# Kernel tuning notes

Measured on AMD Instinct MI355X. Metric: run time of the kernel, lower is better.

Reference implementation:

```python
import jax, jax.numpy as jnp
import numpy as np

B, K, D, H, ZDIM = 65536, 16, 64, 128, 16

def setup_inputs() -> dict:
    key = jax.random.key(0)
    ks = jax.random.split(key, 20)
    s = 0.05
    inp = {
        'z': jax.random.normal(ks[0], (B, ZDIM), dtype=jnp.float32),
        'y': jax.random.randint(ks[1], (B,), 0, K),
        # backbone: 4 fc blocks (Linear+ReLU)
        'bw0': jax.random.normal(ks[2], (ZDIM, H), dtype=jnp.float32) * s,
        'bb0': jnp.zeros((H,), dtype=jnp.float32),
        'bw1': jax.random.normal(ks[3], (H, H), dtype=jnp.float32) * s,
        'bb1': jnp.zeros((H,), dtype=jnp.float32),
        'bw2': jax.random.normal(ks[4], (H, H), dtype=jnp.float32) * s,
        'bb2': jnp.zeros((H,), dtype=jnp.float32),
        'bw3': jax.random.normal(ks[5], (H, H), dtype=jnp.float32) * s,
        'bb3': jnp.zeros((H,), dtype=jnp.float32),
        # K heads, weights stacked on leading expert axis; layers 0-2 have ReLU, layer 3 does not
        'hw0': jax.random.normal(ks[6], (K, H, H), dtype=jnp.float32) * s,
        'hb0': jnp.zeros((K, H), dtype=jnp.float32),
        'hw1': jax.random.normal(ks[7], (K, H, H), dtype=jnp.float32) * s,
        'hb1': jnp.zeros((K, H), dtype=jnp.float32),
        'hw2': jax.random.normal(ks[8], (K, H, H), dtype=jnp.float32) * s,
        'hb2': jnp.zeros((K, H), dtype=jnp.float32),
        'hw3': jax.random.normal(ks[9], (K, H, D), dtype=jnp.float32) * s,
        'hb3': jnp.zeros((K, D), dtype=jnp.float32),
    }
    return inp

def reference(z, y, bw0, bb0, bw1, bb1, bw2, bb2, bw3, bb3,
              hw0, hb0, hw1, hb1, hw2, hb2, hw3, hb3):
    h = jax.nn.relu(z @ bw0 + bb0)
    h = jax.nn.relu(h @ bw1 + bb1)
    h = jax.nn.relu(h @ bw2 + bb2)
    h = jax.nn.relu(h @ bw3 + bb3)          # [B, H]
    # all K expert heads (faithful to original: compute all, then gather)
    a = jax.nn.relu(jnp.einsum('bi,kij->bkj', h, hw0) + hb0)  # [B, K, H]
    a = jax.nn.relu(jnp.einsum('bki,kij->bkj', a, hw1) + hb1)
    a = jax.nn.relu(jnp.einsum('bki,kij->bkj', a, hw2) + hb2)
    a = jnp.einsum('bki,kij->bkj', a, hw3) + hb3              # [B, K, D], no ReLU
    # select the y-th head per sample
    out = jnp.take_along_axis(a, y[:, None, None], axis=1)[:, 0, :]  # [B, D]
    return out
```

## Files before the change

kernel.cpp:

```cpp
#include <hip/hip_runtime.h>
#include <hip/hip_bf16.h>
#include <stdint.h>


typedef _Float16 f16;
typedef __attribute__((ext_vector_type(4)))  _Float16 f16x4;
typedef __attribute__((ext_vector_type(8)))  _Float16 f16x8;
typedef __attribute__((ext_vector_type(16))) float    f32x16;
typedef uint32_t u32;

#define MFMA(a, b, c) __builtin_amdgcn_mfma_f32_32x32x16_f16((a), (b), (c), 0, 0, 0)

constexpr int Bc = 65536;
constexpr int Kc = 16;
constexpr int Hc = 128;
constexpr int Dc = 64;

constexpr int CAP  = 4608;
constexpr int BPE  = CAP / 64;
constexpr int NBLK = Kc * BPE;

constexpr float INV_LOSCALE = 1.0f / 1024.0f;

constexpr int BBW_F16 = 2048 + 3 * 16384;
constexpr int HWE_F16 = 3 * 16384 + 8192;

__device__ __forceinline__ f32x16 zero16() {
    f32x16 z;
#pragma unroll
    for (int i = 0; i < 16; ++i) z[i] = 0.0f;
    return z;
}

__device__ __forceinline__ int actOff(int s, int u) {
    return s * 128 + ((u ^ (s & 15)) << 3);
}

template<bool RELU>
__device__ __forceinline__ void epi_store(
    const f32x16& aH0, const f32x16& aL0,
    const f32x16& aH1, const f32x16& aL1,
    const float* biasLds, f16* aOut, int wid, int l31, int bh)
{
#pragma unroll
    for (int rg = 0; rg < 4; ++rg) {
        const float4 bv = *(const float4*)(biasLds + 32 * wid + 8 * rg + 4 * bh);
        const float bb[4] = {bv.x, bv.y, bv.z, bv.w};
#pragma unroll
        for (int mt = 0; mt < 2; ++mt) {
            const f32x16& aH = mt ? aH1 : aH0;
            const f32x16& aL = mt ? aL1 : aL0;
            f16x4 h4;
#pragma unroll
            for (int j = 0; j < 4; ++j) {
                float v = fmaf(aL[4 * rg + j], INV_LOSCALE, aH[4 * rg + j]) + bb[j];
                if (RELU) v = fmaxf(v, 0.0f);
                h4[j] = (f16)v;
            }
            const int s = 32 * mt + l31;
            *(f16x4*)(aOut + actOff(s, 4 * wid + rg) + 4 * bh) = h4;
        }
    }
}

__device__ __forceinline__ void layer4(
    const f16* __restrict__ Wh, const f16* __restrict__ Wl,
    const float* biasLds, const f16* aIn, f16* aOut,
    int wid, int lane, int l31, int bh)
{
    const f16* ph = Wh + wid * 4096 + lane * 8;
    const f16* pl = Wl + wid * 4096 + lane * 8;

    f32x16 aH0 = zero16(), aH1 = zero16(), aL0 = zero16(), aL1 = zero16();
#pragma unroll
    for (int ks = 0; ks < 8; ++ks) {
        const f16x8 whi = *(const f16x8*)(ph + ks * 512);
        const f16x8 wlo = *(const f16x8*)(pl + ks * 512);
        const f16x8 a0 = *(const f16x8*)(aIn + actOff(l31,      2 * ks + bh));
        const f16x8 a1 = *(const f16x8*)(aIn + actOff(32 + l31, 2 * ks + bh));
        aH0 = MFMA(whi, a0, aH0);
        aH1 = MFMA(whi, a1, aH1);
        aL0 = MFMA(wlo, a0, aL0);
        aL1 = MFMA(wlo, a1, aL1);
    }
    epi_store<true>(aH0, aL0, aH1, aL1, biasLds, aOut, wid, l31, bh);
}

__global__ __launch_bounds__(256, 3) void backbone_mfma(
    const float* __restrict__ z,
    const f16* __restrict__ bbH, const f16* __restrict__ bbL,
    const float* __restrict__ bb0, const float* __restrict__ bb1,
    const float* __restrict__ bb2, const float* __restrict__ bb3,
    f16* __restrict__ hHi)
{
    __shared__ __attribute__((aligned(16))) f16 A[64 * 128];
    __shared__ __attribute__((aligned(16))) f16 B[64 * 128];
    __shared__ __attribute__((aligned(16))) float BIAS[512];

    const int tid = threadIdx.x;
    const int wid = tid >> 6, lane = tid & 63;
    const int l31 = lane & 31, bh = lane >> 5;
    const int s0 = blockIdx.x * 64;

#pragma unroll
    for (int r = 0; r < 2; ++r) {
        const int i = r * 256 + tid;
        float v;
        if      (i < 128) v = bb0[i];
        else if (i < 256) v = bb1[i - 128];
        else if (i < 384) v = bb2[i - 256];
        else              v = bb3[i - 384];
        BIAS[i] = v;
    }

    if (tid < 128) {
        const int m = tid >> 1, hf = tid & 1;
        const float* zp = z + (size_t)(s0 + m) * 16 + hf * 8;
        const float4 a0 = *(const float4*)(zp);
        const float4 a1 = *(const float4*)(zp + 4);
        f16x8 t;
        t[0] = (f16)a0.x; t[1] = (f16)a0.y; t[2] = (f16)a0.z; t[3] = (f16)a0.w;
        t[4] = (f16)a1.x; t[5] = (f16)a1.y; t[6] = (f16)a1.z; t[7] = (f16)a1.w;
        *(f16x8*)(A + actOff(m, hf)) = t;
    }
    __syncthreads();

    {
        const f16x8 w0h = *(const f16x8*)(bbH + wid * 512 + lane * 8);
        const f16x8 w0l = *(const f16x8*)(bbL + wid * 512 + lane * 8);
        const f16x8 a0 = *(const f16x8*)(A + actOff(l31,      bh));
        const f16x8 a1 = *(const f16x8*)(A + actOff(32 + l31, bh));
        f32x16 aH0 = zero16(), aH1 = zero16(), aL0 = zero16(), aL1 = zero16();
        aH0 = MFMA(w0h, a0, aH0);
        aH1 = MFMA(w0h, a1, aH1);
        aL0 = MFMA(w0l, a0, aL0);
        aL1 = MFMA(w0l, a1, aL1);
        epi_store<true>(aH0, aL0, aH1, aL1, BIAS, B, wid, l31, bh);
    }
    __syncthreads();

    layer4(bbH + 2048,  bbL + 2048,  BIAS + 128, B, A, wid, lane, l31, bh);
    __syncthreads();
    layer4(bbH + 18432, bbL + 18432, BIAS + 256, A, B, wid, lane, l31, bh);
    __syncthreads();
    layer4(bbH + 34816, bbL + 34816, BIAS + 384, B, A, wid, lane, l31, bh);
    __syncthreads();

    {
        const int m = tid >> 2, q = tid & 3;
#pragma unroll
        for (int i = 0; i < 4; ++i) {
            const f16x8 v = *(const f16x8*)(A + actOff(m, 4 * q + i));
            *(f16x8*)(hHi + (size_t)(s0 + m) * Hc + q * 32 + i * 8) = v;
        }
    }
}

__global__ void scatter_kernel(const int* __restrict__ y,
                               int* __restrict__ idxb, int* __restrict__ cursor)
{
    __shared__ int lc[Kc];
    __shared__ int lbase[Kc];
    const int tx = threadIdx.x;
    if (tx < Kc) lc[tx] = 0;
    __syncthreads();
    const int b = blockIdx.x * 256 + tx;
    const int e = y[b];
    const int r = atomicAdd(&lc[e], 1);
    __syncthreads();
    if (tx < Kc) lbase[tx] = atomicAdd(&cursor[tx * 16], lc[tx]);
    __syncthreads();
    const int slot = lbase[e] + r;
    if (slot < CAP) idxb[e * CAP + slot] = b;
}

__global__ __launch_bounds__(256, 3) void heads_mfma(
    const f16* hHi,
    const int* __restrict__ idxb, const int* __restrict__ cursor,
    const f16* __restrict__ hH, const f16* __restrict__ hL,
    const float* __restrict__ hb0, const float* __restrict__ hb1,
    const float* __restrict__ hb2, const float* __restrict__ hb3,
    float* out)
{
    __shared__ __attribute__((aligned(16))) f16 A[64 * 128];
    __shared__ __attribute__((aligned(16))) f16 B[64 * 128];
    __shared__ __attribute__((aligned(16))) float BIAS[512];
    __shared__ int sidx[64];

    const int blk = blockIdx.x;
    const int e = blk / BPE;
    const int local0 = (blk % BPE) * 64;
    const int cnt = min(cursor[e * 16], CAP);
    const int nvalid = cnt - local0;
    if (nvalid <= 0) return;

    const int tid = threadIdx.x;
    const int wid = tid >> 6, lane = tid & 63;
    const int l31 = lane & 31, bh = lane >> 5;

#pragma unroll
    for (int r = 0; r < 2; ++r) {
        const int i = r * 256 + tid;
        if (i < 448) {
            float v;
            if      (i < 128) v = hb0[e * Hc + i];
            else if (i < 256) v = hb1[e * Hc + i - 128];
            else if (i < 384) v = hb2[e * Hc + i - 256];
            else              v = hb3[e * Dc + i - 384];
            BIAS[i] = v;
        }
    }
    if (tid < 64) sidx[tid] = (tid < nvalid) ? idxb[e * CAP + local0 + tid] : -1;
    __syncthreads();

    {
        const int m = tid >> 2, q = tid & 3;
        const int b = sidx[m];
        if (b >= 0) {
            const f16* hp = hHi + (size_t)b * Hc + q * 32;
#pragma unroll
            for (int i = 0; i < 4; ++i)
                *(f16x8*)(A + actOff(m, 4 * q + i)) = *(const f16x8*)(hp + i * 8);
        } else {
            f16x8 zz;
#pragma unroll
            for (int j = 0; j < 8; ++j) zz[j] = (f16)0.0f;
#pragma unroll
            for (int i = 0; i < 4; ++i)
                *(f16x8*)(A + actOff(m, 4 * q + i)) = zz;
        }
    }
    __syncthreads();

    const size_t we = (size_t)e * HWE_F16;
    layer4(hH + we,         hL + we,         BIAS,       A, B, wid, lane, l31, bh);
    __syncthreads();
    layer4(hH + we + 16384, hL + we + 16384, BIAS + 128, B, A, wid, lane, l31, bh);
    __syncthreads();
    layer4(hH + we + 32768, hL + we + 32768, BIAS + 256, A, B, wid, lane, l31, bh);
    __syncthreads();

    if (wid < 2) {
        const f16* ph = hH + we + 49152 + wid * 4096 + lane * 8;
        const f16* pl = hL + we + 49152 + wid * 4096 + lane * 8;
        f32x16 aH0 = zero16(), aH1 = zero16(), aL0 = zero16(), aL1 = zero16();
#pragma unroll
        for (int ks = 0; ks < 8; ++ks) {
            const f16x8 whi = *(const f16x8*)(ph + ks * 512);
            const f16x8 wlo = *(const f16x8*)(pl + ks * 512);
            const f16x8 a0 = *(const f16x8*)(B + actOff(l31,      2 * ks + bh));
            const f16x8 a1 = *(const f16x8*)(B + actOff(32 + l31, 2 * ks + bh));
            aH0 = MFMA(whi, a0, aH0);
            aH1 = MFMA(whi, a1, aH1);
            aL0 = MFMA(wlo, a0, aL0);
            aL1 = MFMA(wlo, a1, aL1);
        }
#pragma unroll
        for (int mt = 0; mt < 2; ++mt) {
            const int b = sidx[32 * mt + l31];
            if (b < 0) continue;
            const f32x16& aH = mt ? aH1 : aH0;
            const f32x16& aL = mt ? aL1 : aL0;
#pragma unroll
            for (int rg = 0; rg < 4; ++rg) {
                const int nb = 32 * wid + 8 * rg + 4 * bh;
                const float4 bv = *(const float4*)(BIAS + 384 + nb);
                float4 v;
                v.x = fmaf(aL[4 * rg + 0], INV_LOSCALE, aH[4 * rg + 0]) + bv.x;
                v.y = fmaf(aL[4 * rg + 1], INV_LOSCALE, aH[4 * rg + 1]) + bv.y;
                v.z = fmaf(aL[4 * rg + 2], INV_LOSCALE, aH[4 * rg + 2]) + bv.z;
                v.w = fmaf(aL[4 * rg + 3], INV_LOSCALE, aH[4 * rg + 3]) + bv.w;
                *(float4*)(out + (size_t)b * Dc + nb) = v;
            }
        }
    }
}

__global__ void prep_w(
    const float* __restrict__ bw0, const float* __restrict__ bw1,
    const float* __restrict__ bw2, const float* __restrict__ bw3,
    const float* __restrict__ hw0, const float* __restrict__ hw1,
    const float* __restrict__ hw2, const float* __restrict__ hw3,
    f16* __restrict__ bbH, f16* __restrict__ bbL,
    f16* __restrict__ hH,  f16* __restrict__ hL,
    int* __restrict__ cursor)
{
    __shared__ float T[32][33];
    const int id = blockIdx.x;
    const int tx = threadIdx.x;

    if (id == 0) cursor[tx] = 0;

    const float* src; f16 *dh, *dl;
    int K, N, k0, n0;
    bool big;

    if (id < 52) {
        if (id < 4) {
            src = bw0; dh = bbH; dl = bbL;
            K = 16; N = 128; k0 = 0; n0 = id * 32; big = false;
        } else {
            const int t = id - 4;
            const int l = t / 16, tile = t % 16;
            const float* bws[3] = {bw1, bw2, bw3};
            src = bws[l];
            dh = bbH + 2048 + l * 16384;
            dl = bbL + 2048 + l * 16384;
            K = 128; N = 128; big = true;
            k0 = (tile >> 2) * 32; n0 = (tile & 3) * 32;
        }
    } else {
        const int t = id - 52;
        const int e = t / 56, r = t % 56;
        if (r < 48) {
            const int l = r / 16, tile = r % 16;
            const float* hws[3] = {hw0, hw1, hw2};
            src = hws[l] + (size_t)e * 16384;
            dh = hH + (size_t)e * HWE_F16 + l * 16384;
            dl = hL + (size_t)e * HWE_F16 + l * 16384;
            K = 128; N = 128; big = true;
            k0 = (tile >> 2) * 32; n0 = (tile & 3) * 32;
        } else {
            const int r2 = r - 48;
            src = hw3 + (size_t)e * 8192;
            dh = hH + (size_t)e * HWE_F16 + 49152;
            dl = hL + (size_t)e * HWE_F16 + 49152;
            K = 128; N = 64; big = true;
            k0 = (r2 >> 1) * 32; n0 = (r2 & 1) * 32;
        }
    }

    const int c = tx & 31, g = tx >> 5;
#pragma unroll
    for (int i = 0; i < 4; ++i) {
        const int row = g * 4 + i;
        if (k0 + row < K)
            T[c][row] = src[(size_t)(k0 + row) * N + n0 + c];
    }
    __syncthreads();
#pragma unroll
    for (int i = 0; i < 4; ++i) {
        const int n = n0 + g * 4 + i;
        const int k = k0 + c;
        if (k < K) {
            const float v = T[g * 4 + i][c];
            const f16 hi = (f16)v;
            const f16 lo = (f16)((v - (float)hi) * 1024.0f);
            size_t didx;
            if (big)
                didx = (size_t)(n >> 5) * 4096 + (size_t)(k >> 4) * 512
                     + ((k >> 3) & 1) * 256 + (n & 31) * 8 + (k & 7);
            else
                didx = (size_t)(n >> 5) * 512 + (size_t)(k >> 3) * 256
                     + (n & 31) * 8 + (k & 7);
            dh[didx] = hi;
            dl[didx] = lo;
        }
    }
}

extern "C" void kernel_launch(void* const* d_in, const int* in_sizes, int n_in,
                              void* d_out, int out_size, void* d_ws, size_t ws_size,
                              hipStream_t stream)
{
    const float* z   = (const float*)d_in[0];
    const int*   y   = (const int*)d_in[1];
    const float* bw0 = (const float*)d_in[2];
    const float* bb0 = (const float*)d_in[3];
    const float* bw1 = (const float*)d_in[4];
    const float* bb1 = (const float*)d_in[5];
    const float* bw2 = (const float*)d_in[6];
    const float* bb2 = (const float*)d_in[7];
    const float* bw3 = (const float*)d_in[8];
    const float* bb3 = (const float*)d_in[9];
    const float* hw0 = (const float*)d_in[10];
    const float* hb0 = (const float*)d_in[11];
    const float* hw1 = (const float*)d_in[12];
    const float* hb1 = (const float*)d_in[13];
    const float* hw2 = (const float*)d_in[14];
    const float* hb2 = (const float*)d_in[15];
    const float* hw3 = (const float*)d_in[16];
    const float* hb3 = (const float*)d_in[17];
    float* out = (float*)d_out;

    f16* hHi = (f16*)d_out;

    char* p = (char*)d_ws;
    f16* bbH = (f16*)p;  p += (size_t)BBW_F16 * 2;
    f16* bbL = (f16*)p;  p += (size_t)BBW_F16 * 2;
    f16* hH  = (f16*)p;  p += (size_t)Kc * HWE_F16 * 2;
    f16* hL  = (f16*)p;  p += (size_t)Kc * HWE_F16 * 2;
    int* idxb = (int*)p; p += (size_t)Kc * CAP * 4;
    int* cursor = (int*)p;

    prep_w<<<52 + Kc * 56, 256, 0, stream>>>(bw0, bw1, bw2, bw3,
                                             hw0, hw1, hw2, hw3,
                                             bbH, bbL, hH, hL, cursor);

    scatter_kernel<<<Bc / 256, 256, 0, stream>>>(y, idxb, cursor);

    backbone_mfma<<<Bc / 64, 256, 0, stream>>>(z, bbH, bbL,
                                               bb0, bb1, bb2, bb3, hHi);

    heads_mfma<<<NBLK, 256, 0, stream>>>(hHi, idxb, cursor,
                                         hH, hL, hb0, hb1, hb2, hb3, out);
}
```

Baseline: 154.1 us.

## Fuse backbone and head MLPs into one expert-grouped kernel, merge prep with scatter

The backbone and the selected head now run in one kernel. Samples are gathered by expert up front, so each block loads z rows by index, runs the four backbone layers and then that expert's head layers entirely in LDS. This removes the f16 hidden-state round trip through global memory and one kernel launch. The weight-prep and scatter kernels are merged into a single grid, with the cursor cleared by a memset, to cut another launch. The risk is that per-block bias loads grow, and samples beyond CAP per expert are still dropped as before.

```diff
diff --git a/kernel.cpp b/kernel.cpp
--- a/kernel.cpp
+++ b/kernel.cpp
@@ -24,6 +24,8 @@
 
 constexpr int BBW_F16 = 2048 + 3 * 16384;
 constexpr int HWE_F16 = 3 * 16384 + 8192;
+
+constexpr int PREP_BLKS = 52 + Kc * 56;
 
 __device__ __forceinline__ f32x16 zero16() {
     f32x16 z;
@@ -86,42 +88,63 @@
     epi_store<true>(aH0, aL0, aH1, aL1, biasLds, aOut, wid, l31, bh);
 }
 
-__global__ __launch_bounds__(256, 3) void backbone_mfma(
+__global__ __launch_bounds__(256, 3) void fused_mlp(
     const float* __restrict__ z,
+    const int* __restrict__ idxb, const int* __restrict__ cursor,
     const f16* __restrict__ bbH, const f16* __restrict__ bbL,
     const float* __restrict__ bb0, const float* __restrict__ bb1,
     const float* __restrict__ bb2, const float* __restrict__ bb3,
-    f16* __restrict__ hHi)
+    const f16* __restrict__ hH, const f16* __restrict__ hL,
+    const float* __restrict__ hb0, const float* __restrict__ hb1,
+    const float* __restrict__ hb2, const float* __restrict__ hb3,
+    float* __restrict__ out)
 {
     __shared__ __attribute__((aligned(16))) f16 A[64 * 128];
     __shared__ __attribute__((aligned(16))) f16 B[64 * 128];
-    __shared__ __attribute__((aligned(16))) float BIAS[512];
+    __shared__ __attribute__((aligned(16))) float BIAS[960];
+    __shared__ int sidx[64];
+
+    const int blk = blockIdx.x;
+    const int e = blk / BPE;
+    const int local0 = (blk % BPE) * 64;
+    const int cnt = min(cursor[e * 16], CAP);
+    const int nvalid = cnt - local0;
+    if (nvalid <= 0) return;
 
     const int tid = threadIdx.x;
     const int wid = tid >> 6, lane = tid & 63;
     const int l31 = lane & 31, bh = lane >> 5;
-    const int s0 = blockIdx.x * 64;
-
-#pragma unroll
-    for (int r = 0; r < 2; ++r) {
+
+#pragma unroll
+    for (int r = 0; r < 4; ++r) {
         const int i = r * 256 + tid;
-        float v;
-        if      (i < 128) v = bb0[i];
-        else if (i < 256) v = bb1[i - 128];
-        else if (i < 384) v = bb2[i - 256];
-        else              v = bb3[i - 384];
-        BIAS[i] = v;
-    }
-
-    if (tid < 128) {
-        const int m = tid >> 1, hf = tid & 1;
-        const float* zp = z + (size_t)(s0 + m) * 16 + hf * 8;
-        const float4 a0 = *(const float4*)(zp);
-        const float4 a1 = *(const float4*)(zp + 4);
-        f16x8 t;
-        t[0] = (f16)a0.x; t[1] = (f16)a0.y; t[2] = (f16)a0.z; t[3] = (f16)a0.w;
-        t[4] = (f16)a1.x; t[5] = (f16)a1.y; t[6] = (f16)a1.z; t[7] = (f16)a1.w;
-        *(f16x8*)(A + actOff(m, hf)) = t;
+        if (i < 960) {
+            float v;
+            if      (i < 128) v = bb0[i];
+            else if (i < 256) v = bb1[i - 128];
+            else if (i < 384) v = bb2[i - 256];
+            else if (i < 512) v = bb3[i - 384];
+            else if (i < 640) v = hb0[e * Hc + i - 512];
+            else if (i < 768) v = hb1[e * Hc + i - 640];
+            else if (i < 896) v = hb2[e * Hc + i - 768];
+            else              v = hb3[e * Dc + i - 896];
+            BIAS[i] = v;
+        }
+    }
+    if (tid < 64) sidx[tid] = (tid < nvalid) ? idxb[e * CAP + local0 + tid] : -1;
+    __syncthreads();
+
+    {
+        const int m = tid >> 2, q = tid & 3;
+        const int b = sidx[m];
+        f16x4 t;
+        if (b >= 0) {
+            const float4 v = *(const float4*)(z + (size_t)b * 16 + q * 4);
+            t[0] = (f16)v.x; t[1] = (f16)v.y; t[2] = (f16)v.z; t[3] = (f16)v.w;
+        } else {
+            t[0] = t[1] = t[2] = t[3] = (f16)0.0f;
+        }
+        *(f16x4*)(A + actOff(m, q >> 1) + (q & 1) * 4) = t;
     }
     __syncthreads();
 
@@ -146,98 +169,12 @@
     layer4(bbH + 34816, bbL + 34816, BIAS + 384, B, A, wid, lane, l31, bh);
     __syncthreads();
 
-    {
-        const int m = tid >> 2, q = tid & 3;
-#pragma unroll
-        for (int i = 0; i < 4; ++i) {
-            const f16x8 v = *(const f16x8*)(A + actOff(m, 4 * q + i));
-            *(f16x8*)(hHi + (size_t)(s0 + m) * Hc + q * 32 + i * 8) = v;
-        }
-    }
-}
-
-__global__ void scatter_kernel(const int* __restrict__ y,
-                               int* __restrict__ idxb, int* __restrict__ cursor)
-{
-    __shared__ int lc[Kc];
-    __shared__ int lbase[Kc];
-    const int tx = threadIdx.x;
-    if (tx < Kc) lc[tx] = 0;
-    __syncthreads();
-    const int b = blockIdx.x * 256 + tx;
-    const int e = y[b];
-    const int r = atomicAdd(&lc[e], 1);
-    __syncthreads();
-    if (tx < Kc) lbase[tx] = atomicAdd(&cursor[tx * 16], lc[tx]);
-    __syncthreads();
-    const int slot = lbase[e] + r;
-    if (slot < CAP) idxb[e * CAP + slot] = b;
-}
-
-__global__ __launch_bounds__(256, 3) void heads_mfma(
-    const f16* hHi,
-    const int* __restrict__ idxb, const int* __restrict__ cursor,
-    const f16* __restrict__ hH, const f16* __restrict__ hL,
-    const float* __restrict__ hb0, const float* __restrict__ hb1,
-    const float* __restrict__ hb2, const float* __restrict__ hb3,
-    float* out)
-{
-    __shared__ __attribute__((aligned(16))) f16 A[64 * 128];
-    __shared__ __attribute__((aligned(16))) f16 B[64 * 128];
-    __shared__ __attribute__((aligned(16))) float BIAS[512];
-    __shared__ int sidx[64];
-
-    const int blk = blockIdx.x;
-    const int e = blk / BPE;
-    const int local0 = (blk % BPE) * 64;
-    const int cnt = min(cursor[e * 16], CAP);
-    const int nvalid = cnt - local0;
-    if (nvalid <= 0) return;
-
-    const int tid = threadIdx.x;
-    const int wid = tid >> 6, lane = tid & 63;
-    const int l31 = lane & 31, bh = lane >> 5;
-
-#pragma unroll
-    for (int r = 0; r < 2; ++r) {
-        const int i = r * 256 + tid;
-        if (i < 448) {
-            float v;
-            if      (i < 128) v = hb0[e * Hc + i];
-            else if (i < 256) v = hb1[e * Hc + i - 128];
-            else if (i < 384) v = hb2[e * Hc + i - 256];
-            else              v = hb3[e * Dc + i - 384];
-            BIAS[i] = v;
-        }
-    }
-    if (tid < 64) sidx[tid] = (tid < nvalid) ? idxb[e * CAP + local0 + tid] : -1;
-    __syncthreads();
-
-    {
-        const int m = tid >> 2, q = tid & 3;
-        const int b = sidx[m];
-        if (b >= 0) {
-            const f16* hp = hHi + (size_t)b * Hc + q * 32;
-#pragma unroll
-            for (int i = 0; i < 4; ++i)
-                *(f16x8*)(A + actOff(m, 4 * q + i)) = *(const f16x8*)(hp + i * 8);
-        } else {
-            f16x8 zz;
-#pragma unroll
-            for (int j = 0; j < 8; ++j) zz[j] = (f16)0.0f;
-#pragma unroll
-            for (int i = 0; i < 4; ++i)
-                *(f16x8*)(A + actOff(m, 4 * q + i)) = zz;
-        }
-    }
-    __syncthreads();
-
     const size_t we = (size_t)e * HWE_F16;
-    layer4(hH + we,         hL + we,         BIAS,       A, B, wid, lane, l31, bh);
-    __syncthreads();
-    layer4(hH + we + 16384, hL + we + 16384, BIAS + 128, B, A, wid, lane, l31, bh);
-    __syncthreads();
-    layer4(hH + we + 32768, hL + we + 32768, BIAS + 256, A, B, wid, lane, l31, bh);
+    layer4(hH + we,         hL + we,         BIAS + 512, A, B, wid, lane, l31, bh);
+    __syncthreads();
+    layer4(hH + we + 16384, hL + we + 16384, BIAS + 640, B, A, wid, lane, l31, bh);
+    __syncthreads();
+    layer4(hH + we + 32768, hL + we + 32768, BIAS + 768, A, B, wid, lane, l31, bh);
     __syncthreads();
 
     if (wid < 2) {
@@ -264,7 +201,7 @@
 #pragma unroll
             for (int rg = 0; rg < 4; ++rg) {
                 const int nb = 32 * wid + 8 * rg + 4 * bh;
-                const float4 bv = *(const float4*)(BIAS + 384 + nb);
+                const float4 bv = *(const float4*)(BIAS + 896 + nb);
                 float4 v;
                 v.x = fmaf(aL[4 * rg + 0], INV_LOSCALE, aH[4 * rg + 0]) + bv.x;
                 v.y = fmaf(aL[4 * rg + 1], INV_LOSCALE, aH[4 * rg + 1]) + bv.y;
@@ -276,20 +213,34 @@
     }
 }
 
-__global__ void prep_w(
+__global__ void prep_scatter(
     const float* __restrict__ bw0, const float* __restrict__ bw1,
     const float* __restrict__ bw2, const float* __restrict__ bw3,
     const float* __restrict__ hw0, const float* __restrict__ hw1,
     const float* __restrict__ hw2, const float* __restrict__ hw3,
     f16* __restrict__ bbH, f16* __restrict__ bbL,
     f16* __restrict__ hH,  f16* __restrict__ hL,
-    int* __restrict__ cursor)
+    const int* __restrict__ y, int* __restrict__ idxb, int* __restrict__ cursor)
 {
     __shared__ float T[32][33];
+    __shared__ int lc[Kc];
+    __shared__ int lbase[Kc];
     const int id = blockIdx.x;
     const int tx = threadIdx.x;
 
-    if (id == 0) cursor[tx] = 0;
+    if (id >= PREP_BLKS) {
+        if (tx < Kc) lc[tx] = 0;
+        __syncthreads();
+        const int b = (id - PREP_BLKS) * 256 + tx;
+        const int e = y[b];
+        const int r = atomicAdd(&lc[e], 1);
+        __syncthreads();
+        if (tx < Kc) lbase[tx] = atomicAdd(&cursor[tx * 16], lc[tx]);
+        __syncthreads();
+        const int slot = lbase[e] + r;
+        if (slot < CAP) idxb[e * CAP + slot] = b;
+        return;
+    }
 
     const float* src; f16 *dh, *dl;
     int K, N, k0, n0;
@@ -383,8 +334,6 @@
     const float* hb3 = (const float*)d_in[17];
     float* out = (float*)d_out;
 
-    f16* hHi = (f16*)d_out;
-
     char* p = (char*)d_ws;
     f16* bbH = (f16*)p;  p += (size_t)BBW_F16 * 2;
     f16* bbL = (f16*)p;  p += (size_t)BBW_F16 * 2;
@@ -393,15 +342,13 @@
     int* idxb = (int*)p; p += (size_t)Kc * CAP * 4;
     int* cursor = (int*)p;
 
-    prep_w<<<52 + Kc * 56, 256, 0, stream>>>(bw0, bw1, bw2, bw3,
-                                             hw0, hw1, hw2, hw3,
-                                             bbH, bbL, hH, hL, cursor);
-
-    scatter_kernel<<<Bc / 256, 256, 0, stream>>>(y, idxb, cursor);
-
-    backbone_mfma<<<Bc / 64, 256, 0, stream>>>(z, bbH, bbL,
-                                               bb0, bb1, bb2, bb3, hHi);
-
-    heads_mfma<<<NBLK, 256, 0, stream>>>(hHi, idxb, cursor,
-                                         hH, hL, hb0, hb1, hb2, hb3, out);
-}
+    hipMemsetAsync(cursor, 0, 256 * sizeof(int), stream);
+
+    prep_scatter<<<PREP_BLKS + Bc / 256, 256, 0, stream>>>(
+        bw0, bw1, bw2, bw3, hw0, hw1, hw2, hw3,
+        bbH, bbL, hH, hL, y, idxb, cursor);
+
+    fused_mlp<<<NBLK, 256, 0, stream>>>(
+        z, idxb, cursor, bbH, bbL, bb0, bb1, bb2, bb3,
+        hH, hL, hb0, hb1, hb2, hb3, out);
+}
```

After: 151.3 us. No clear change (-1.8%).
